# Kernel tuning notes

Hardware: AMD Instinct MI355X
Metric: run time of the kernel (lower is better)

The kernel has to match this reference:

```python
import jax, jax.numpy as jnp
import numpy as np

N = 4096

def setup_inputs() -> dict:
    key = jax.random.key(0)
    kA, kB = jax.random.split(key)
    # A and B are upper-triangular inputs, as the module assumes
    A = jnp.triu(jax.random.normal(kA, (N, N), dtype=jnp.float32))
    B = jnp.triu(jax.random.normal(kB, (N, N), dtype=jnp.float32))
    return {"A": A, "B": B}

def reference(A, B):
    # C = triu(A @ B); product of upper-triangular matrices is upper-triangular,
    # the kernel additionally masks the lower triangle of the output.
    return jnp.triu(A @ B)
```

## Files before the change

kernel.cpp:

```cpp
#include <hip/hip_runtime.h>


#define N   4096
#define NB  32
#define BM  128
#define BK  32

typedef __attribute__((ext_vector_type(8))) __bf16 bf16x8;
typedef __attribute__((ext_vector_type(4))) float  floatx4;

typedef const __attribute__((address_space(1))) void* gas_ptr;
typedef __attribute__((address_space(3))) void*       las_ptr;

__device__ __forceinline__ unsigned short f32_to_bf16_rne(float f) {
    unsigned u = __builtin_bit_cast(unsigned, f);
    unsigned r = u + 0x7fffu + ((u >> 16) & 1u);
    return (unsigned short)(r >> 16);
}

__global__ void conv_a_kernel(const float* __restrict__ A,
                              unsigned short* __restrict__ Ab) {
    int idx = (blockIdx.x * 256 + threadIdx.x) * 4;
    const float4 v = *(const float4*)(A + idx);
    ushort4 o;
    o.x = f32_to_bf16_rne(v.x);
    o.y = f32_to_bf16_rne(v.y);
    o.z = f32_to_bf16_rne(v.z);
    o.w = f32_to_bf16_rne(v.w);
    *(ushort4*)(Ab + idx) = o;
}

__global__ void conv_bt_kernel(const float* __restrict__ B,
                               unsigned short* __restrict__ Bt) {
    __shared__ float tile[32][33];
    int j0 = blockIdx.x * 32;
    int k0 = blockIdx.y * 32;
    int tx = threadIdx.x;
    int ty = threadIdx.y;
    for (int i = 0; i < 32; i += 8)
        tile[ty + i][tx] = B[(size_t)(k0 + ty + i) * N + j0 + tx];
    __syncthreads();
    for (int i = 0; i < 32; i += 8)
        Bt[(size_t)(j0 + ty + i) * N + k0 + tx] = f32_to_bf16_rne(tile[tx][ty + i]);
}

__global__ __launch_bounds__(256)
void trimm_kernel(const unsigned short* __restrict__ Ab,
                  const unsigned short* __restrict__ Bt,
                  float* __restrict__ C) {
    __shared__ unsigned short sA[BM * BK];
    __shared__ unsigned short sB[BM * BK];

    const int bj = blockIdx.x;
    const int bi = blockIdx.y;

    const int tid  = threadIdx.x;
    const int w    = tid >> 6;
    const int lane = tid & 63;
    const int quad = lane >> 4;
    const int l15  = lane & 15;

    const int m0 = (w >> 1) * 64;
    const int n0 = (w & 1) * 64;
    const int row0 = bi * BM;
    const int col0 = bj * BM;

    floatx4 acc[4][4] = {};

    if (bj >= bi) {
        const int ksteps = (bj - bi + 1) * (BM / BK);
        const int kbase  = bi * BM;

        const int srow = lane >> 2;
        const int skk  = (lane & 3) * 8;

        for (int s = 0; s < ksteps; ++s) {
            const int k0 = kbase + s * BK;
            for (int c = 0; c < 2; ++c) {
                const int q = w * 2 + c;
                const int r = q * 16 + srow;
                const unsigned short* gA = Ab + (size_t)(row0 + r) * N + k0 + skk;
                const unsigned short* gB = Bt + (size_t)(col0 + r) * N + k0 + skk;
                __builtin_amdgcn_global_load_lds((gas_ptr)gA, (las_ptr)&sA[q * 512], 16, 0, 0);
                __builtin_amdgcn_global_load_lds((gas_ptr)gB, (las_ptr)&sB[q * 512], 16, 0, 0);
            }
            __syncthreads();

            bf16x8 af[4], bfr[4];
            #pragma unroll
            for (int t = 0; t < 4; ++t) {
                af[t]  = *(const bf16x8*)&sA[(m0 + t * 16 + l15) * BK + quad * 8];
                bfr[t] = *(const bf16x8*)&sB[(n0 + t * 16 + l15) * BK + quad * 8];
            }
            #pragma unroll
            for (int tm = 0; tm < 4; ++tm)
                #pragma unroll
                for (int tn = 0; tn < 4; ++tn)
                    acc[tm][tn] = __builtin_amdgcn_mfma_f32_16x16x32_bf16(
                        af[tm], bfr[tn], acc[tm][tn], 0, 0, 0);
            __syncthreads();
        }
    }

    #pragma unroll
    for (int tm = 0; tm < 4; ++tm) {
        const int grow_base = row0 + m0 + tm * 16 + quad * 4;
        #pragma unroll
        for (int tn = 0; tn < 4; ++tn) {
            const int gcol = col0 + n0 + tn * 16 + l15;
            #pragma unroll
            for (int r = 0; r < 4; ++r) {
                const int grow = grow_base + r;
                const float v = (gcol >= grow) ? acc[tm][tn][r] : 0.0f;
                C[(size_t)grow * N + gcol] = v;
            }
        }
    }
}

extern "C" void kernel_launch(void* const* d_in, const int* in_sizes, int n_in,
                              void* d_out, int out_size, void* d_ws, size_t ws_size,
                              hipStream_t stream) {
    const float* A = (const float*)d_in[0];
    const float* B = (const float*)d_in[1];
    float* C = (float*)d_out;

    unsigned short* Ab = (unsigned short*)d_ws;
    unsigned short* Bt = Ab + (size_t)N * N;

    conv_a_kernel<<<dim3(N * N / 1024), dim3(256), 0, stream>>>(A, Ab);
    conv_bt_kernel<<<dim3(N / 32, N / 32), dim3(32, 8), 0, stream>>>(B, Bt);
    trimm_kernel<<<dim3(NB, NB), dim3(256), 0, stream>>>(Ab, Bt, C);
}
```

Baseline: 270.7 us.

## Load-balance triangular GEMM with split-K over diagonals and skip lower-triangle conversion

Replaces the full 32x32 grid, where lower-triangle blocks did no work, with a 1D grid that maps only upper-triangle tiles. Long diagonals are split along K into chunks combined with atomicAdd, after the output is zeroed by a memset. The A and B conversion kernels now skip blocks that the GEMM never reads, and the B transpose uses 64x64 tiles with vectorised loads and stores. Possible costs are atomic traffic on the split tiles, the added memset, and a nondeterministic summation order.

```diff
diff --git a/kernel.cpp b/kernel.cpp
--- a/kernel.cpp
+++ b/kernel.cpp
@@ -5,9 +5,12 @@
 #define NB  32
 #define BM  128
 #define BK  32
+#define CH  8
+#define NWG 1000
 
 typedef __attribute__((ext_vector_type(8))) __bf16 bf16x8;
 typedef __attribute__((ext_vector_type(4))) float  floatx4;
+typedef __attribute__((ext_vector_type(8))) unsigned short ushort8;
 
 typedef const __attribute__((address_space(1))) void* gas_ptr;
 typedef __attribute__((address_space(3))) void*       las_ptr;
@@ -20,7 +23,12 @@
 
 __global__ void conv_a_kernel(const float* __restrict__ A,
                               unsigned short* __restrict__ Ab) {
-    int idx = (blockIdx.x * 256 + threadIdx.x) * 4;
+    const int bid = blockIdx.x;
+    const int row = bid >> 2;
+    const int k0  = (bid & 3) * 1024;
+    const int rb  = row >> 7;
+    if (((k0 >> 7) + 8) <= rb) return;
+    const int idx = row * N + k0 + threadIdx.x * 4;
     const float4 v = *(const float4*)(A + idx);
     ushort4 o;
     o.x = f32_to_bf16_rne(v.x);
@@ -32,16 +40,39 @@
 
 __global__ void conv_bt_kernel(const float* __restrict__ B,
                                unsigned short* __restrict__ Bt) {
-    __shared__ float tile[32][33];
-    int j0 = blockIdx.x * 32;
-    int k0 = blockIdx.y * 32;
-    int tx = threadIdx.x;
-    int ty = threadIdx.y;
-    for (int i = 0; i < 32; i += 8)
-        tile[ty + i][tx] = B[(size_t)(k0 + ty + i) * N + j0 + tx];
+    __shared__ float tile[64][65];
+    const int jb = blockIdx.x;
+    const int kb = blockIdx.y;
+    if ((kb >> 1) > (jb >> 1)) return;
+    const int j0 = jb * 64, k0 = kb * 64;
+    const int t  = threadIdx.x;
+    {
+        const int kl = t >> 2;
+        const int j4 = (t & 3) * 16;
+        const float* src = B + (size_t)(k0 + kl) * N + j0 + j4;
+        const float4 v0 = ((const float4*)src)[0];
+        const float4 v1 = ((const float4*)src)[1];
+        const float4 v2 = ((const float4*)src)[2];
+        const float4 v3 = ((const float4*)src)[3];
+        float* dst = &tile[kl][j4];
+        dst[0]=v0.x; dst[1]=v0.y; dst[2]=v0.z; dst[3]=v0.w;
+        dst[4]=v1.x; dst[5]=v1.y; dst[6]=v1.z; dst[7]=v1.w;
+        dst[8]=v2.x; dst[9]=v2.y; dst[10]=v2.z; dst[11]=v2.w;
+        dst[12]=v3.x; dst[13]=v3.y; dst[14]=v3.z; dst[15]=v3.w;
+    }
     __syncthreads();
-    for (int i = 0; i < 32; i += 8)
-        Bt[(size_t)(j0 + ty + i) * N + k0 + tx] = f32_to_bf16_rne(tile[tx][ty + i]);
+    {
+        const int jl = t >> 2;
+        const int k4 = (t & 3) * 16;
+        ushort8 o0, o1;
+        #pragma unroll
+        for (int i = 0; i < 8; ++i) o0[i] = f32_to_bf16_rne(tile[k4 + i][jl]);
+        #pragma unroll
+        for (int i = 0; i < 8; ++i) o1[i] = f32_to_bf16_rne(tile[k4 + 8 + i][jl]);
+        unsigned short* dst = Bt + (size_t)(j0 + jl) * N + k0 + k4;
+        ((ushort8*)dst)[0] = o0;
+        ((ushort8*)dst)[1] = o1;
+    }
 }
 
 __global__ __launch_bounds__(256)
@@ -51,8 +82,21 @@
     __shared__ unsigned short sA[BM * BK];
     __shared__ unsigned short sB[BM * BK];
 
-    const int bj = blockIdx.x;
-    const int bi = blockIdx.y;
+    int rem = blockIdx.x;
+    int d = 0, per = 1;
+    for (int dd = NB - 1; dd >= 0; --dd) {
+        const int p   = (dd + CH) / CH;
+        const int cnt = (NB - dd) * p;
+        if (rem < cnt) { d = dd; per = p; break; }
+        rem -= cnt;
+    }
+    const int tile  = rem / per;
+    const int chunk = rem - tile * per;
+    const int bi = tile, bj = tile + d;
+    const int c    = d + 1;
+    const int base = c / per, extra = c - base * per;
+    const int kb0  = bi + chunk * base + (chunk < extra ? chunk : extra);
+    const int len  = base + (chunk < extra ? 1 : 0);
 
     const int tid  = threadIdx.x;
     const int w    = tid >> 6;
@@ -67,39 +111,36 @@
 
     floatx4 acc[4][4] = {};
 
-    if (bj >= bi) {
-        const int ksteps = (bj - bi + 1) * (BM / BK);
-        const int kbase  = bi * BM;
+    const int srow = lane >> 2;
+    const int skk  = (lane & 3) * 8;
 
-        const int srow = lane >> 2;
-        const int skk  = (lane & 3) * 8;
+    const int s0 = kb0 * 4;
+    const int ns = len * 4;
+    for (int s = 0; s < ns; ++s) {
+        const int k0 = (s0 + s) * BK;
+        for (int cc = 0; cc < 2; ++cc) {
+            const int q = w * 2 + cc;
+            const int r = q * 16 + srow;
+            const unsigned short* gA = Ab + (size_t)(row0 + r) * N + k0 + skk;
+            const unsigned short* gB = Bt + (size_t)(col0 + r) * N + k0 + skk;
+            __builtin_amdgcn_global_load_lds((gas_ptr)gA, (las_ptr)&sA[q * 512], 16, 0, 0);
+            __builtin_amdgcn_global_load_lds((gas_ptr)gB, (las_ptr)&sB[q * 512], 16, 0, 0);
+        }
+        __syncthreads();
 
-        for (int s = 0; s < ksteps; ++s) {
-            const int k0 = kbase + s * BK;
-            for (int c = 0; c < 2; ++c) {
-                const int q = w * 2 + c;
-                const int r = q * 16 + srow;
-                const unsigned short* gA = Ab + (size_t)(row0 + r) * N + k0 + skk;
-                const unsigned short* gB = Bt + (size_t)(col0 + r) * N + k0 + skk;
-                __builtin_amdgcn_global_load_lds((gas_ptr)gA, (las_ptr)&sA[q * 512], 16, 0, 0);
-                __builtin_amdgcn_global_load_lds((gas_ptr)gB, (las_ptr)&sB[q * 512], 16, 0, 0);
-            }
-            __syncthreads();
-
-            bf16x8 af[4], bfr[4];
+        bf16x8 af[4], bfr[4];
+        #pragma unroll
+        for (int t = 0; t < 4; ++t) {
+            af[t]  = *(const bf16x8*)&sA[(m0 + t * 16 + l15) * BK + quad * 8];
+            bfr[t] = *(const bf16x8*)&sB[(n0 + t * 16 + l15) * BK + quad * 8];
+        }
+        #pragma unroll
+        for (int tm = 0; tm < 4; ++tm)
             #pragma unroll
-            for (int t = 0; t < 4; ++t) {
-                af[t]  = *(const bf16x8*)&sA[(m0 + t * 16 + l15) * BK + quad * 8];
-                bfr[t] = *(const bf16x8*)&sB[(n0 + t * 16 + l15) * BK + quad * 8];
-            }
-            #pragma unroll
-            for (int tm = 0; tm < 4; ++tm)
-                #pragma unroll
-                for (int tn = 0; tn < 4; ++tn)
-                    acc[tm][tn] = __builtin_amdgcn_mfma_f32_16x16x32_bf16(
-                        af[tm], bfr[tn], acc[tm][tn], 0, 0, 0);
-            __syncthreads();
-        }
+            for (int tn = 0; tn < 4; ++tn)
+                acc[tm][tn] = __builtin_amdgcn_mfma_f32_16x16x32_bf16(
+                    af[tm], bfr[tn], acc[tm][tn], 0, 0, 0);
+        __syncthreads();
     }
 
     #pragma unroll
@@ -111,8 +152,15 @@
             #pragma unroll
             for (int r = 0; r < 4; ++r) {
                 const int grow = grow_base + r;
-                const float v = (gcol >= grow) ? acc[tm][tn][r] : 0.0f;
-                C[(size_t)grow * N + gcol] = v;
+                float* p = C + (size_t)grow * N + gcol;
+                const float v = acc[tm][tn][r];
+                if (per > 1) {
+                    atomicAdd(p, v);
+                } else if (d != 0) {
+                    *p = v;
+                } else if (gcol >= grow) {
+                    *p = v;
+                }
             }
         }
     }
@@ -128,7 +176,8 @@
     unsigned short* Ab = (unsigned short*)d_ws;
     unsigned short* Bt = Ab + (size_t)N * N;
 
-    conv_a_kernel<<<dim3(N * N / 1024), dim3(256), 0, stream>>>(A, Ab);
-    conv_bt_kernel<<<dim3(N / 32, N / 32), dim3(32, 8), 0, stream>>>(B, Bt);
-    trimm_kernel<<<dim3(NB, NB), dim3(256), 0, stream>>>(Ab, Bt, C);
+    hipMemsetAsync(d_out, 0, (size_t)N * N * sizeof(float), stream);
+    conv_a_kernel<<<dim3(N * 4), dim3(256), 0, stream>>>(A, Ab);
+    conv_bt_kernel<<<dim3(N / 64, N / 64), dim3(256), 0, stream>>>(B, Bt);
+    trimm_kernel<<<dim3(NWG), dim3(256), 0, stream>>>(Ab, Bt, C);
 }
```

After: 251.5 us. -7.1%, faster.
